# Performance work log

Hardware: AMD Instinct MI355X
Metric: run time of the kernel (lower is better)

## Reference

```python
import jax, jax.numpy as jnp
import numpy as np

N, E, DIM, L, NPERM, B = 20000, 640000, 128, 4, 20000, 256
R = NPERM * L * L  # rows of perm matrices
EPS = 1e-5


def _mlp(x, w1, b1, g, beta, w2, b2):
    # Linear -> BatchNorm (training-mode batch stats) -> ReLU -> Linear
    h = x @ w1 + b1
    mu = h.mean(0)
    var = h.var(0)  # biased, matches torch BN normalization
    h = (h - mu) * jax.lax.rsqrt(var + EPS) * g + beta
    return jax.nn.relu(h) @ w2 + b2


def setup_inputs() -> dict:
    key = jax.random.key(0)
    ks = jax.random.split(key, 40)
    s = 0.05
    inp = {}
    inp["node_feat"] = jax.random.normal(ks[0], (N, DIM), jnp.float32)
    inp["edge_feat"] = jax.random.normal(ks[1], (E, DIM), jnp.float32)
    inp["src"] = jax.random.randint(ks[2], (E,), 0, N)
    inp["dst"] = jax.random.randint(ks[3], (E,), 0, N)
    inp["rev_flag"] = jax.random.randint(ks[4], (E,), 0, 2).astype(bool)
    # sparse node_to_perm / edge_to_perm: one nnz per row (row i implicit)
    inp["n2p_cols"] = jax.random.randint(ks[5], (R,), 0, N)
    inp["n2p_vals"] = jax.random.uniform(ks[6], (R,), jnp.float32)
    inp["e2p_cols"] = jax.random.randint(ks[7], (R,), 0, E)
    inp["e2p_vals"] = jax.random.uniform(ks[8], (R,), jnp.float32)
    # sparse pooling matrix: perm j -> graph pool_rows[j] with weight pool_vals[j]
    inp["pool_rows"] = jax.random.randint(ks[9], (NPERM,), 0, B)
    inp["pool_vals"] = jax.random.uniform(ks[10], (NPERM,), jnp.float32)
    for i, n in enumerate(["in_w", "out_w", "src_w", "dst_w", "nloop_w", "eloop_w"]):
        inp[n] = jax.random.normal(ks[11 + i], (DIM, DIM), jnp.float32) * s
    inp["lrp_w"] = jax.random.normal(ks[17], (DIM, DIM, L * L), jnp.float32) * s
    inp["nbias"] = jnp.zeros((DIM,), jnp.float32)
    inp["ebias"] = jnp.zeros((DIM,), jnp.float32)
    inp["lrp_bias"] = jnp.zeros((DIM,), jnp.float32)
    for p, k0 in (("n", 20), ("e", 26)):
        inp[p + "mlp_w1"] = jax.random.normal(ks[k0], (DIM, DIM), jnp.float32) * s
        inp[p + "mlp_b1"] = jnp.zeros((DIM,), jnp.float32)
        inp[p + "mlp_g"] = jnp.ones((DIM,), jnp.float32)
        inp[p + "mlp_beta"] = jnp.zeros((DIM,), jnp.float32)
        inp[p + "mlp_w2"] = jax.random.normal(ks[k0 + 1], (DIM, DIM), jnp.float32) * s
        inp[p + "mlp_b2"] = jnp.zeros((DIM,), jnp.float32)
    return inp


def reference(node_feat, edge_feat, src, dst, rev_flag, n2p_cols, n2p_vals,
              e2p_cols, e2p_vals, pool_rows, pool_vals,
              in_w, out_w, src_w, dst_w, nloop_w, eloop_w, lrp_w,
              nbias, ebias, lrp_bias,
              nmlp_w1, nmlp_b1, nmlp_g, nmlp_beta, nmlp_w2, nmlp_b2,
              emlp_w1, emlp_b1, emlp_g, emlp_beta, emlp_w2, emlp_b2):
    hs = node_feat[src]   # [E, d]
    hd = node_feat[dst]   # [E, d]
    r = rev_flag[:, None]
    # per-edge messages with reverse-edge masking
    edge_msg = jnp.where(r, hs @ dst_w - hd @ src_w, hd @ dst_w - hs @ src_w)
    node_msg = jnp.where(r, edge_feat @ out_w, -(edge_feat @ in_w))
    node_agg = jax.ops.segment_sum(node_msg, dst, num_segments=N)
    # node update
    nout = _mlp(node_feat @ nloop_w + node_agg + nbias,
                nmlp_w1, nmlp_b1, nmlp_g, nmlp_beta, nmlp_w2, nmlp_b2)
    # edge update: degree-scaled term uses out-degree of dst node
    out_deg = jax.ops.segment_sum(jnp.ones((E,), jnp.float32), src, num_segments=N)
    dlog = jnp.log2(1.0 + out_deg[dst])[:, None]
    add = 2.0 * (1.0 + dlog) * (edge_feat @ (src_w - dst_w))
    eout = _mlp(edge_feat @ eloop_w + add + edge_msg + ebias,
                emlp_w1, emlp_b1, emlp_g, emlp_beta, emlp_w2, emlp_b2)
    # sparse perm gathers + LRP einsum + sparse pooling scatter
    perm = n2p_vals[:, None] * nout[n2p_cols] + e2p_vals[:, None] * eout[e2p_cols]
    perm = perm.reshape(NPERM, L * L, DIM)
    lrp = jnp.einsum('dab,bca->dc', perm, lrp_w) + lrp_bias
    pooled = jax.ops.segment_sum(pool_vals[:, None] * lrp, pool_rows, num_segments=B)
    return pooled, eout
```

## Files before the change

kernel.cpp:

```cpp
#include <hip/hip_runtime.h>
#include <stdint.h>

constexpr int Nn     = 20000;
constexpr int Ee     = 640000;
constexpr int NPERMc = 20000;

using bf16x8 = __attribute__((ext_vector_type(8))) short;
using f32x4  = __attribute__((ext_vector_type(4))) float;
using s16x4  = __attribute__((ext_vector_type(4))) short;
using u16x8  = __attribute__((ext_vector_type(8))) unsigned short;

__device__ __forceinline__ short f2bf(float f) {
  union { float f; unsigned u; } v; v.f = f;
  unsigned r = v.u + 0x7FFFu + ((v.u >> 16) & 1u);
  return (short)(r >> 16);
}
__device__ __forceinline__ float bf2f(unsigned short s) {
  union { unsigned u; float f; } v; v.u = ((unsigned)s) << 16;
  return v.f;
}
__device__ __forceinline__ f32x4 MFMA(bf16x8 a, bf16x8 b, f32x4 c) {
  return __builtin_amdgcn_mfma_f32_16x16x32_bf16(a, b, c, 0, 0, 0);
}

__device__ __forceinline__ int swz(int s) { return s ^ (((s >> 7) & 7) << 3); }

__device__ __forceinline__ int fragIdx(int k, int n) {
  int t = n >> 4, kk = k >> 5;
  int l = ((k & 31) >> 3) * 16 + (n & 15);
  int j = k & 7;
  return ((t * 4 + kk) * 64 + l) * 8 + j;
}

__device__ __forceinline__ void stage16x128(const float* __restrict__ src, int row0, int M,
                                            int lane, short* lds) {
  #pragma unroll
  for (int it = 0; it < 8; ++it) {
    int u = it * 64 + lane;
    int r = u >> 5;
    int q = u & 31;
    int row = row0 + r;
    float4 v = make_float4(0.f, 0.f, 0.f, 0.f);
    if (row < M) v = ((const float4*)(src + (size_t)row * 128))[q];
    int k  = q * 4;
    int kk = k >> 5;
    int l2 = ((k & 31) >> 3) * 16 + r;
    int j  = k & 7;
    s16x4 s4 = { f2bf(v.x), f2bf(v.y), f2bf(v.z), f2bf(v.w) };
    *(s16x4*)(lds + swz((kk * 64 + l2) * 8 + j)) = s4;
  }
}

__global__ __launch_bounds__(256) void kPrep(
    const float* __restrict__ in_w,  const float* __restrict__ out_w,
    const float* __restrict__ src_w, const float* __restrict__ dst_w,
    const float* __restrict__ nloop_w, const float* __restrict__ eloop_w,
    const float* __restrict__ lrp_w,
    const float* __restrict__ nbias, const float* __restrict__ ebias,
    const float* __restrict__ w1e, const float* __restrict__ b1e,
    const float* __restrict__ w1n, const float* __restrict__ b1n,
    const float* __restrict__ w2e, const float* __restrict__ w2n,
    short* __restrict__ WA, short* __restrict__ BQ, short* __restrict__ WN,
    short* __restrict__ W2E, short* __restrict__ W2N, short* __restrict__ WL,
    float* __restrict__ c0e, float* __restrict__ c0n) {
  __shared__ float Rl[16384];
  int tid = threadIdx.x;
  int blk = blockIdx.x;
  if (blk < 448) {
    int p = blk >> 6, sub = blk & 63;
    const float* La; const float* Lb = nullptr; const float* R; short* outp;
    float sOut = 1.f;
    switch (p) {
      case 0: La = eloop_w;             R = w1e; outp = WA;          break;
      case 1: La = src_w; Lb = dst_w;   R = w1e; outp = WA + 16384;  break;
      case 2: La = dst_w;               R = w1e; outp = BQ;          break;
      case 3: La = src_w;               R = w1e; outp = BQ + 16384;  break;
      case 4: La = nloop_w;             R = w1n; outp = WN;          break;
      case 5: La = out_w;               R = w1n; outp = WN + 16384;  break;
      default: La = in_w;               R = w1n; outp = WN + 32768; sOut = -1.f; break;
    }
    for (int i = tid; i < 16384; i += 256) Rl[i] = R[i];
    __syncthreads();
    int e = sub * 256 + tid;
    int k = e >> 7, n = e & 127;
    float acc = 0.f;
    bool hasLb = (Lb != nullptr);
    for (int j = 0; j < 128; ++j) {
      float l = La[k * 128 + j];
      if (hasLb) l -= Lb[k * 128 + j];
      acc += l * Rl[j * 128 + n];
    }
    outp[fragIdx(k, n)] = f2bf(acc * sOut);
  } else if (blk < 512) {
    int e = (blk - 448) * 256 + tid; int k = e >> 7, n = e & 127;
    W2E[fragIdx(k, n)] = f2bf(w2e[k * 128 + n]);
  } else if (blk < 576) {
    int e = (blk - 512) * 256 + tid; int k = e >> 7, n = e & 127;
    W2N[fragIdx(k, n)] = f2bf(w2n[k * 128 + n]);
  } else if (blk < 1600) {
    int q = blk - 576; int a = q >> 6;
    int e = (q & 63) * 256 + tid; int k = e >> 7, n = e & 127;
    WL[a * 16384 + fragIdx(k, n)] = f2bf(lrp_w[(k * 128 + n) * 16 + a]);
  } else {
    if (tid < 128) {
      float acc = 0.f;
      for (int k2 = 0; k2 < 128; ++k2) acc += ebias[k2] * w1e[k2 * 128 + tid];
      c0e[tid] = acc + b1e[tid];
    } else {
      int n = tid - 128; float acc = 0.f;
      for (int k2 = 0; k2 < 128; ++k2) acc += nbias[k2] * w1n[k2 * 128 + n];
      c0n[n] = acc + b1n[n];
    }
  }
}


__global__ __launch_bounds__(256) void kHist(
    const int* __restrict__ srcI, const int* __restrict__ dstI,
    int* __restrict__ cnt, float* __restrict__ deg) {
  int e = blockIdx.x * 256 + threadIdx.x;
  atomicAdd(&cnt[dstI[e]], 1);
  atomicAdd(&deg[srcI[e]], 1.0f);
}

__global__ __launch_bounds__(256) void kScan(const int* __restrict__ cnt,
                                             int* __restrict__ off,
                                             int* __restrict__ cur) {
  __shared__ int lc[Nn];
  __shared__ int ps[256];
  int tid = threadIdx.x;
  for (int i = tid; i < Nn; i += 256) lc[i] = cnt[i];
  __syncthreads();
  constexpr int CH = (Nn + 255) / 256;
  int base = tid * CH;
  int local = 0;
  for (int i = 0; i < CH; ++i) {
    int idx = base + i;
    if (idx < Nn) local += lc[idx];
  }
  ps[tid] = local;
  __syncthreads();
  for (int d = 1; d < 256; d <<= 1) {
    int t = (tid >= d) ? ps[tid - d] : 0;
    __syncthreads();
    if (tid >= d) ps[tid] += t;
    __syncthreads();
  }
  int run = ps[tid] - local;
  for (int i = 0; i < CH; ++i) {
    int idx = base + i;
    if (idx < Nn) { off[idx] = run; cur[idx] = run; run += lc[idx]; }
  }
}

__global__ __launch_bounds__(256) void kScatter(
    const int* __restrict__ dstI, const int* __restrict__ revI,
    int* __restrict__ cur, int* __restrict__ order) {
  int e = blockIdx.x * 256 + threadIdx.x;
  int pos = atomicAdd(&cur[dstI[e]], 1);
  order[pos] = revI[e] ? (e | (int)0x80000000) : e;
}

__global__ __launch_bounds__(256) void kAgg2(
    const float* __restrict__ ef, const int* __restrict__ off,
    const int* __restrict__ cnt, const int* __restrict__ order,
    float* __restrict__ aggR, float* __restrict__ aggN) {
  int w = threadIdx.x >> 6, lane = threadIdx.x & 63;
  int n = blockIdx.x * 4 + w;
  if (n >= Nn) return;
  int s0 = off[n], c = cnt[n];
  float2 aR = make_float2(0.f, 0.f), aN = make_float2(0.f, 0.f);
  int i = 0;
  for (; i + 3 < c; i += 4) {
    int oe0 = order[s0 + i];
    int oe1 = order[s0 + i + 1];
    int oe2 = order[s0 + i + 2];
    int oe3 = order[s0 + i + 3];
    float2 v0 = ((const float2*)(ef + (size_t)(oe0 & 0x7fffffff) * 128))[lane];
    float2 v1 = ((const float2*)(ef + (size_t)(oe1 & 0x7fffffff) * 128))[lane];
    float2 v2 = ((const float2*)(ef + (size_t)(oe2 & 0x7fffffff) * 128))[lane];
    float2 v3 = ((const float2*)(ef + (size_t)(oe3 & 0x7fffffff) * 128))[lane];
    if (oe0 < 0) { aR.x += v0.x; aR.y += v0.y; } else { aN.x += v0.x; aN.y += v0.y; }
    if (oe1 < 0) { aR.x += v1.x; aR.y += v1.y; } else { aN.x += v1.x; aN.y += v1.y; }
    if (oe2 < 0) { aR.x += v2.x; aR.y += v2.y; } else { aN.x += v2.x; aN.y += v2.y; }
    if (oe3 < 0) { aR.x += v3.x; aR.y += v3.y; } else { aN.x += v3.x; aN.y += v3.y; }
  }
  for (; i < c; ++i) {
    int oe = order[s0 + i];
    int e = oe & 0x7fffffff;
    float2 v = ((const float2*)(ef + (size_t)e * 128))[lane];
    if (oe < 0) { aR.x += v.x; aR.y += v.y; } else { aN.x += v.x; aN.y += v.y; }
  }
  ((float2*)(aggR + (size_t)n * 128))[lane] = aR;
  ((float2*)(aggN + (size_t)n * 128))[lane] = aN;
}

__global__ __launch_bounds__(256, 2) void kQ(const float* __restrict__ nf,
                                             const short* __restrict__ BQ,
                                             float* __restrict__ Q, int M) {
  __shared__ __align__(16) short alds[4][2048];
  __shared__ __align__(16) short wbuf[8192];
  int tid = threadIdx.x, w = tid >> 6, lane = tid & 63;
  int row0 = blockIdx.x * 64 + w * 16;
  stage16x128(nf, row0, M, lane, alds[w]);
  f32x4 acc[16];
  #pragma unroll
  for (int t = 0; t < 16; ++t) acc[t] = (f32x4){0.f, 0.f, 0.f, 0.f};
  const int4* g4 = (const int4*)BQ;
  for (int kk = 0; kk < 4; ++kk) {
    __syncthreads();
    for (int c = tid; c < 1024; c += 256) {
      int t = c >> 6, l = c & 63;
      ((int4*)wbuf)[c] = g4[(t * 4 + kk) * 64 + l];
    }
    __syncthreads();
    bf16x8 a = *(const bf16x8*)(alds[w] + swz((kk * 64 + lane) * 8));
    #pragma unroll
    for (int t = 0; t < 16; ++t) {
      bf16x8 b = *(const bf16x8*)(wbuf + (t * 64 + lane) * 8);
      acc[t] = MFMA(a, b, acc[t]);
    }
  }
  int sub = lane >> 4, m = lane & 15;
  #pragma unroll
  for (int i = 0; i < 4; ++i) {
    int row = row0 + sub * 4 + i;
    if (row < M) {
      #pragma unroll
      for (int h = 0; h < 2; ++h) {
        float4 f0, f1;
        f0.x = acc[h * 8 + 0][i]; f0.y = acc[h * 8 + 1][i];
        f0.z = acc[h * 8 + 2][i]; f0.w = acc[h * 8 + 3][i];
        f1.x = acc[h * 8 + 4][i]; f1.y = acc[h * 8 + 5][i];
        f1.z = acc[h * 8 + 6][i]; f1.w = acc[h * 8 + 7][i];
        float4* dst = (float4*)(Q + (size_t)row * 256 + h * 128 + m * 8);
        dst[0] = f0; dst[1] = f1;
      }
    }
  }
}

__global__ __launch_bounds__(256, 2) void kN1(
    const float* __restrict__ nf, const float* __restrict__ aggR,
    const float* __restrict__ aggN, const short* __restrict__ WN,
    const float* __restrict__ c0n, short* __restrict__ hN,
    float* __restrict__ scratchN, int M) {
  __shared__ __align__(16) short alds[4][2048];
  __shared__ __align__(16) short wlds[16384];
  __shared__ float statsLDS[256];
  int tid = threadIdx.x, w = tid >> 6, lane = tid & 63;
  int m = lane & 15, sub = lane >> 4;
  statsLDS[tid] = 0.f;
  int row0 = blockIdx.x * 64 + w * 16;
  f32x4 acc[8];
  #pragma unroll
  for (int t = 0; t < 8; ++t) acc[t] = (f32x4){0.f, 0.f, 0.f, 0.f};
  for (int s = 0; s < 3; ++s) {
    const float* src = (s == 0) ? nf : ((s == 1) ? aggR : aggN);
    __syncthreads();
    const int4* g4 = (const int4*)(WN + s * 16384);
    for (int c = tid; c < 2048; c += 256) ((int4*)wlds)[c] = g4[c];
    __syncthreads();
    stage16x128(src, row0, M, lane, alds[w]);
    for (int kk = 0; kk < 4; ++kk) {
      bf16x8 a = *(const bf16x8*)(alds[w] + swz((kk * 64 + lane) * 8));
      #pragma unroll
      for (int t = 0; t < 8; ++t) {
        bf16x8 b = *(const bf16x8*)(wlds + ((t * 4 + kk) * 64 + lane) * 8);
        acc[t] = MFMA(a, b, acc[t]);
      }
    }
  }
  float c0v[8];
  #pragma unroll
  for (int t = 0; t < 8; ++t) c0v[t] = c0n[t * 16 + m];
  float ss[8], sq[8];
  #pragma unroll
  for (int t = 0; t < 8; ++t) { ss[t] = 0.f; sq[t] = 0.f; }
  #pragma unroll
  for (int i = 0; i < 4; ++i) {
    int row = row0 + sub * 4 + i;
    if (row < M) {
      bf16x8 pk;
      #pragma unroll
      for (int t = 0; t < 8; ++t) {
        float h = acc[t][i] + c0v[t];
        pk[t] = f2bf(h); ss[t] += h; sq[t] += h * h;
      }
      *(bf16x8*)(hN + (size_t)row * 128 + m * 8) = pk;
    }
  }
  #pragma unroll
  for (int t = 0; t < 8; ++t) {
    float a = ss[t], b = sq[t];
    a += __shfl_xor(a, 16, 64); b += __shfl_xor(b, 16, 64);
    a += __shfl_xor(a, 32, 64); b += __shfl_xor(b, 32, 64);
    if (lane < 16) {
      atomicAdd(&statsLDS[t * 16 + lane], a);
      atomicAdd(&statsLDS[128 + t * 16 + lane], b);
    }
  }
  __syncthreads();
  scratchN[(size_t)tid * gridDim.x + blockIdx.x] = statsLDS[tid];
}

__global__ __launch_bounds__(256, 4) void kD(
    const float* __restrict__ ef, const short* __restrict__ WA,
    const float* __restrict__ Q, const float* __restrict__ c0e,
    const int* __restrict__ srcI, const int* __restrict__ dstI,
    const int* __restrict__ revI, const float* __restrict__ deg,
    short* __restrict__ hE, float* __restrict__ scratchE) {
  __shared__ __align__(16) short alds[4][2048];
  __shared__ __align__(16) short wbuf[8192];
  __shared__ float statsLDS[256];
  int tid = threadIdx.x, w = tid >> 6, lane = tid & 63;
  int m = lane & 15, sub = lane >> 4;
  statsLDS[tid] = 0.f;
  int row0 = blockIdx.x * 64 + w * 16;
  float scl[4]; int qa[4], qb[4];
  #pragma unroll
  for (int i = 0; i < 4; ++i) {
    int e = row0 + sub * 4 + i;
    int s_ = srcI[e], d_ = dstI[e], r_ = revI[e];
    scl[i] = 2.0f * (1.0f + log2f(1.0f + deg[d_]));
    int na = r_ ? s_ : d_;
    int nb = r_ ? d_ : s_;
    qa[i] = na * 256 + m * 8;
    qb[i] = nb * 256 + 128 + m * 8;
  }
  stage16x128(ef, row0, Ee, lane, alds[w]);
  f32x4 acc1[8], acc2[8];
  #pragma unroll
  for (int t = 0; t < 8; ++t) { acc1[t] = (f32x4){0,0,0,0}; acc2[t] = (f32x4){0,0,0,0}; }
  const int4* g4 = (const int4*)WA;
  for (int kk = 0; kk < 4; ++kk) {
    __syncthreads();
    for (int c = tid; c < 1024; c += 256) {
      int mm = c >> 9, t = (c >> 6) & 7, l = c & 63;
      ((int4*)wbuf)[c] = g4[mm * 2048 + (t * 4 + kk) * 64 + l];
    }
    __syncthreads();
    bf16x8 a = *(const bf16x8*)(alds[w] + swz((kk * 64 + lane) * 8));
    #pragma unroll
    for (int t = 0; t < 8; ++t) {
      bf16x8 b1 = *(const bf16x8*)(wbuf + (t * 64 + lane) * 8);
      bf16x8 b2 = *(const bf16x8*)(wbuf + 4096 + (t * 64 + lane) * 8);
      acc1[t] = MFMA(a, b1, acc1[t]);
      acc2[t] = MFMA(a, b2, acc2[t]);
    }
  }
  float c0v[8];
  #pragma unroll
  for (int t = 0; t < 8; ++t) c0v[t] = c0e[t * 16 + m];
  float ss[8], sq[8];
  #pragma unroll
  for (int t = 0; t < 8; ++t) { ss[t] = 0.f; sq[t] = 0.f; }
  #pragma unroll
  for (int i = 0; i < 4; ++i) {
    int e = row0 + sub * 4 + i;
    float4 A0 = ((const float4*)(Q + qa[i]))[0];
    float4 A1 = ((const float4*)(Q + qa[i]))[1];
    float4 B0 = ((const float4*)(Q + qb[i]))[0];
    float4 B1 = ((const float4*)(Q + qb[i]))[1];
    float qv[8] = {A0.x - B0.x, A0.y - B0.y, A0.z - B0.z, A0.w - B0.w,
                   A1.x - B1.x, A1.y - B1.y, A1.z - B1.z, A1.w - B1.w};
    bf16x8 pk;
    #pragma unroll
    for (int t = 0; t < 8; ++t) {
      float h = acc1[t][i] + scl[i] * acc2[t][i] + qv[t] + c0v[t];
      pk[t] = f2bf(h);
      ss[t] += h; sq[t] += h * h;
    }
    *(bf16x8*)(hE + (size_t)e * 128 + m * 8) = pk;
  }
  #pragma unroll
  for (int t = 0; t < 8; ++t) {
    float a = ss[t], b = sq[t];
    a += __shfl_xor(a, 16, 64); b += __shfl_xor(b, 16, 64);
    a += __shfl_xor(a, 32, 64); b += __shfl_xor(b, 32, 64);
    if (lane < 16) {
      atomicAdd(&statsLDS[t * 16 + lane], a);
      atomicAdd(&statsLDS[128 + t * 16 + lane], b);
    }
  }
  __syncthreads();
  scratchE[(size_t)tid * gridDim.x + blockIdx.x] = statsLDS[tid];
}

__global__ __launch_bounds__(256) void kFin(const float* __restrict__ scratch, int NB,
                                            float M, const float* __restrict__ g,
                                            const float* __restrict__ beta,
                                            float* __restrict__ st) {
  __shared__ float red[256];
  __shared__ float red2[256];
  int c = blockIdx.x;
  int tid = threadIdx.x;
  float s = 0.f, q = 0.f;
  for (int i = tid; i < NB; i += 256) {
    s += scratch[(size_t)c * NB + i];
    q += scratch[(size_t)(128 + c) * NB + i];
  }
  red[tid] = s; red2[tid] = q;
  __syncthreads();
  for (int off = 128; off > 0; off >>= 1) {
    if (tid < off) { red[tid] += red[tid + off]; red2[tid] += red2[tid + off]; }
    __syncthreads();
  }
  if (tid == 0) {
    float mu  = red[0] / M;
    float var = red2[0] / M - mu * mu;
    float inv = rsqrtf(var + 1e-5f);
    float sc  = g[c] * inv;
    st[c] = sc;
    st[128 + c] = beta[c] - mu * sc;
  }
}

__global__ __launch_bounds__(256, 2) void kF(const short* __restrict__ h,
                                             const float* __restrict__ st,
                                             const short* __restrict__ w2f,
                                             const float* __restrict__ b2,
                                             float* __restrict__ outp, int M) {
  __shared__ __align__(16) short alds[4][2048];
  __shared__ __align__(16) short wlds[16384];
  int tid = threadIdx.x, w = tid >> 6, lane = tid & 63;
  int m2 = lane & 15;
  for (int c = tid; c < 2048; c += 256) ((int4*)wlds)[c] = ((const int4*)w2f)[c];
  int row0 = blockIdx.x * 64 + w * 16;
  float sc8[8], tb8[8];
  #pragma unroll
  for (int q = 0; q < 8; ++q) {
    int col = q * 16 + m2;
    sc8[q] = st[col]; tb8[q] = st[128 + col];
  }
  #pragma unroll
  for (int it = 0; it < 4; ++it) {
    int r = it * 4 + (lane >> 4);
    int row = row0 + r;
    u16x8 hv = {0, 0, 0, 0, 0, 0, 0, 0};
    if (row < M) hv = *(const u16x8*)(h + (size_t)row * 128 + m2 * 8);
    #pragma unroll
    for (int q = 0; q < 8; ++q) {
      float f = bf2f(hv[q]);
      float v = fmaxf(f * sc8[q] + tb8[q], 0.f);
      int k = q * 16 + m2;
      int kk = k >> 5, l2 = ((k & 31) >> 3) * 16 + r, j = k & 7;
      alds[w][swz((kk * 64 + l2) * 8 + j)] = f2bf(v);
    }
  }
  __syncthreads();
  f32x4 acc[8];
  #pragma unroll
  for (int t = 0; t < 8; ++t) acc[t] = (f32x4){0.f, 0.f, 0.f, 0.f};
  for (int kk = 0; kk < 4; ++kk) {
    bf16x8 a = *(const bf16x8*)(alds[w] + swz((kk * 64 + lane) * 8));
    #pragma unroll
    for (int t = 0; t < 8; ++t) {
      bf16x8 b = *(const bf16x8*)(wlds + ((t * 4 + kk) * 64 + lane) * 8);
      acc[t] = MFMA(a, b, acc[t]);
    }
  }
  int sub = lane >> 4;
  #pragma unroll
  for (int t = 0; t < 8; ++t) {
    int col = t * 16 + (lane & 15);
    float bb = b2[col];
    #pragma unroll
    for (int i = 0; i < 4; ++i) {
      int row = row0 + sub * 4 + i;
      if (row < M) outp[(size_t)row * 128 + col] = acc[t][i] + bb;
    }
  }
}

__global__ __launch_bounds__(256, 2) void kLRP(
    const float* __restrict__ nout, const float* __restrict__ eoutp,
    const int* __restrict__ n2pc, const float* __restrict__ n2pv,
    const int* __restrict__ e2pc, const float* __restrict__ e2pv,
    const int* __restrict__ poolr, const float* __restrict__ poolv,
    const short* __restrict__ WL, const float* __restrict__ lrp_bias,
    float* __restrict__ pooled) {
  __shared__ __align__(16) short alds[4][2048];
  __shared__ __align__(16) short wlds[16384];
  int tid = threadIdx.x, w = tid >> 6, lane = tid & 63;
  int blk = blockIdx.x % 313, g = blockIdx.x / 313;
  int row0 = blk * 64 + w * 16;
  int a0 = g * 4;
  f32x4 acc[8];
  #pragma unroll
  for (int t = 0; t < 8; ++t) acc[t] = (f32x4){0.f, 0.f, 0.f, 0.f};
  for (int a = a0; a < a0 + 4; ++a) {
    __syncthreads();
    const int4* g4 = (const int4*)(WL + a * 16384);
    for (int c = tid; c < 2048; c += 256) ((int4*)wlds)[c] = g4[c];
    __syncthreads();
    #pragma unroll
    for (int it = 0; it < 8; ++it) {
      int u = it * 64 + lane;
      int r = u >> 5;
      int q = u & 31;
      int d = row0 + r;
      float4 v = make_float4(0.f, 0.f, 0.f, 0.f);
      if (d < NPERMc) {
        int i = d * 16 + a;
        int nc = n2pc[i]; float nv = n2pv[i];
        int ec = e2pc[i]; float ev = e2pv[i];
        float4 nr = ((const float4*)(nout  + (size_t)nc * 128))[q];
        float4 er = ((const float4*)(eoutp + (size_t)ec * 128))[q];
        v.x = nv * nr.x + ev * er.x;
        v.y = nv * nr.y + ev * er.y;
        v.z = nv * nr.z + ev * er.z;
        v.w = nv * nr.w + ev * er.w;
      }
      int k  = q * 4;
      int kk = k >> 5;
      int l2 = ((k & 31) >> 3) * 16 + r;
      int j  = k & 7;
      s16x4 s4 = { f2bf(v.x), f2bf(v.y), f2bf(v.z), f2bf(v.w) };
      *(s16x4*)(alds[w] + swz((kk * 64 + l2) * 8 + j)) = s4;
    }
    for (int kk = 0; kk < 4; ++kk) {
      bf16x8 aa = *(const bf16x8*)(alds[w] + swz((kk * 64 + lane) * 8));
      #pragma unroll
      for (int t = 0; t < 8; ++t) {
        bf16x8 b = *(const bf16x8*)(wlds + ((t * 4 + kk) * 64 + lane) * 8);
        acc[t] = MFMA(aa, b, acc[t]);
      }
    }
  }
  int sub = lane >> 4;
  #pragma unroll
  for (int t = 0; t < 8; ++t) {
    int col = t * 16 + (lane & 15);
    float lb = (g == 0) ? lrp_bias[col] : 0.f;
    #pragma unroll
    for (int i = 0; i < 4; ++i) {
      int d = row0 + sub * 4 + i;
      if (d < NPERMc) {
        float val = acc[t][i] + lb;
        atomicAdd(&pooled[poolr[d] * 128 + col], poolv[d] * val);
      }
    }
  }
}

extern "C" void kernel_launch(void* const* d_in, const int* in_sizes, int n_in,
                              void* d_out, int out_size, void* d_ws, size_t ws_size,
                              hipStream_t stream) {
  (void)in_sizes; (void)n_in; (void)out_size; (void)ws_size;
  const float* node_feat = (const float*)d_in[0];
  const float* edge_feat = (const float*)d_in[1];
  const int*   srcI      = (const int*)d_in[2];
  const int*   dstI      = (const int*)d_in[3];
  const int*   revI      = (const int*)d_in[4];
  const int*   n2pc      = (const int*)d_in[5];
  const float* n2pv      = (const float*)d_in[6];
  const int*   e2pc      = (const int*)d_in[7];
  const float* e2pv      = (const float*)d_in[8];
  const int*   poolr     = (const int*)d_in[9];
  const float* poolv     = (const float*)d_in[10];
  const float* in_w      = (const float*)d_in[11];
  const float* out_w     = (const float*)d_in[12];
  const float* src_w     = (const float*)d_in[13];
  const float* dst_w     = (const float*)d_in[14];
  const float* nloop_w   = (const float*)d_in[15];
  const float* eloop_w   = (const float*)d_in[16];
  const float* lrp_w     = (const float*)d_in[17];
  const float* nbias     = (const float*)d_in[18];
  const float* ebias     = (const float*)d_in[19];
  const float* lrp_bias  = (const float*)d_in[20];
  const float* nmlp_w1   = (const float*)d_in[21];
  const float* nmlp_b1   = (const float*)d_in[22];
  const float* nmlp_g    = (const float*)d_in[23];
  const float* nmlp_beta = (const float*)d_in[24];
  const float* nmlp_w2   = (const float*)d_in[25];
  const float* nmlp_b2   = (const float*)d_in[26];
  const float* emlp_w1   = (const float*)d_in[27];
  const float* emlp_b1   = (const float*)d_in[28];
  const float* emlp_g    = (const float*)d_in[29];
  const float* emlp_beta = (const float*)d_in[30];
  const float* emlp_w2   = (const float*)d_in[31];
  const float* emlp_b2   = (const float*)d_in[32];

  float* pooled = (float*)d_out;
  float* eoutp  = (float*)d_out + 32768;

  char* p = (char*)d_ws;
  auto alloc = [&](size_t b) { char* r = p; p += (b + 255) & ~(size_t)255; return r; };
  short* hE   = (short*)alloc((size_t)Ee * 128 * 2);
  float* Qm   = (float*)alloc((size_t)Nn * 256 * 4);
  float* aggR = (float*)alloc((size_t)Nn * 128 * 4);
  float* aggN = (float*)alloc((size_t)Nn * 128 * 4);
  short* hN   = (short*)alloc((size_t)Nn * 128 * 2);
  float* nout = (float*)alloc((size_t)Nn * 128 * 4);
  float* deg  = (float*)alloc((size_t)Nn * 4);
  float* scrE = (float*)alloc((size_t)256 * 10000 * 4);
  float* scrN = (float*)alloc((size_t)256 * 313 * 4);
  float* stE  = (float*)alloc(256 * 4);
  float* stN  = (float*)alloc(256 * 4);
  short* WA   = (short*)alloc(32768 * 2);
  short* BQ   = (short*)alloc(32768 * 2);
  short* WN   = (short*)alloc(49152 * 2);
  short* W2E  = (short*)alloc(16384 * 2);
  short* W2N  = (short*)alloc(16384 * 2);
  short* WL   = (short*)alloc((size_t)16 * 16384 * 2);
  float* c0e  = (float*)alloc(128 * 4);
  float* c0n  = (float*)alloc(128 * 4);
  int*   cnt  = (int*)alloc((size_t)Nn * 4);
  int*   offA = (int*)alloc((size_t)Nn * 4);
  int*   cur  = (int*)alloc((size_t)Nn * 4);
  int*   order= (int*)alloc((size_t)Ee * 4);

  hipMemsetAsync(deg,  0, (size_t)Nn * 4, stream);
  hipMemsetAsync(cnt,  0, (size_t)Nn * 4, stream);
  hipMemsetAsync(pooled, 0, (size_t)32768 * 4, stream);

  kPrep<<<1601, 256, 0, stream>>>(in_w, out_w, src_w, dst_w, nloop_w, eloop_w, lrp_w,
                                  nbias, ebias, emlp_w1, emlp_b1, nmlp_w1, nmlp_b1,
                                  emlp_w2, nmlp_w2, WA, BQ, WN, W2E, W2N, WL, c0e, c0n);
  kHist<<<Ee / 256, 256, 0, stream>>>(srcI, dstI, cnt, deg);
  kScan<<<1, 256, 0, stream>>>(cnt, offA, cur);
  kScatter<<<Ee / 256, 256, 0, stream>>>(dstI, revI, cur, order);
  kAgg2<<<Nn / 4, 256, 0, stream>>>(edge_feat, offA, cnt, order, aggR, aggN);
  kQ<<<313, 256, 0, stream>>>(node_feat, BQ, Qm, Nn);
  kN1<<<313, 256, 0, stream>>>(node_feat, aggR, aggN, WN, c0n, hN, scrN, Nn);
  kD<<<10000, 256, 0, stream>>>(edge_feat, WA, Qm, c0e, srcI, dstI, revI, deg, hE, scrE);
  kFin<<<128, 256, 0, stream>>>(scrE, 10000, (float)Ee, emlp_g, emlp_beta, stE);
  kFin<<<128, 256, 0, stream>>>(scrN, 313, (float)Nn, nmlp_g, nmlp_beta, stN);
  kF<<<10000, 256, 0, stream>>>(hE, stE, W2E, emlp_b2, eoutp, Ee);
  kF<<<313, 256, 0, stream>>>(hN, stN, W2N, nmlp_b2, nout, Nn);
  kLRP<<<1252, 256, 0, stream>>>(nout, eoutp, n2pc, n2pv, e2pc, e2pv,
                                 poolr, poolv, WL, lrp_bias, pooled);
}
```

Before: 1.358 ms.

## Stream weight tiles per k-step in kF/kLRP and restructure BN stat reduction

kF and kLRP now stage only the 8 KB weight slice for each k-step into a small LDS buffer instead of the full 32 KB weight matrix. This cuts LDS use enough to raise the launch bounds occupancy hints (kF 2→6, kLRP 2→4). The cost is extra barriers and repeated global/L2 reads of the weights per k-step. Separately, per-block BN statistics are now written block-major (coalesced) and reduced by a new two-stage kRed+kFin pass instead of strided column reads.

```diff
diff --git a/kernel.cpp b/kernel.cpp
--- a/kernel.cpp
+++ b/kernel.cpp
@@ -301,7 +301,7 @@
     }
   }
   __syncthreads();
-  scratchN[(size_t)tid * gridDim.x + blockIdx.x] = statsLDS[tid];
+  scratchN[(size_t)blockIdx.x * 256 + tid] = statsLDS[tid];
 }
 
 __global__ __launch_bounds__(256, 4) void kD(
@@ -384,10 +384,19 @@
     }
   }
   __syncthreads();
-  scratchE[(size_t)tid * gridDim.x + blockIdx.x] = statsLDS[tid];
-}
-
-__global__ __launch_bounds__(256) void kFin(const float* __restrict__ scratch, int NB,
+  scratchE[(size_t)blockIdx.x * 256 + tid] = statsLDS[tid];
+}
+
+__global__ __launch_bounds__(256) void kRed(const float* __restrict__ scr, int NB,
+                                            float* __restrict__ part) {
+  int tid = threadIdx.x, b = blockIdx.x;
+  float acc = 0.f;
+  for (int r = b; r < NB; r += 64)
+    acc += scr[(size_t)r * 256 + tid];
+  part[b * 256 + tid] = acc;
+}
+
+__global__ __launch_bounds__(256) void kFin(const float* __restrict__ part,
                                             float M, const float* __restrict__ g,
                                             const float* __restrict__ beta,
                                             float* __restrict__ st) {
@@ -396,13 +405,13 @@
   int c = blockIdx.x;
   int tid = threadIdx.x;
   float s = 0.f, q = 0.f;
-  for (int i = tid; i < NB; i += 256) {
-    s += scratch[(size_t)c * NB + i];
-    q += scratch[(size_t)(128 + c) * NB + i];
+  if (tid < 64) {
+    s = part[tid * 256 + c];
+    q = part[tid * 256 + 128 + c];
   }
   red[tid] = s; red2[tid] = q;
   __syncthreads();
-  for (int off = 128; off > 0; off >>= 1) {
+  for (int off = 32; off > 0; off >>= 1) {
     if (tid < off) { red[tid] += red[tid + off]; red2[tid] += red2[tid + off]; }
     __syncthreads();
   }
@@ -416,16 +425,15 @@
   }
 }
 
-__global__ __launch_bounds__(256, 2) void kF(const short* __restrict__ h,
+__global__ __launch_bounds__(256, 6) void kF(const short* __restrict__ h,
                                              const float* __restrict__ st,
                                              const short* __restrict__ w2f,
                                              const float* __restrict__ b2,
                                              float* __restrict__ outp, int M) {
   __shared__ __align__(16) short alds[4][2048];
-  __shared__ __align__(16) short wlds[16384];
+  __shared__ __align__(16) short wbuf[4096];
   int tid = threadIdx.x, w = tid >> 6, lane = tid & 63;
   int m2 = lane & 15;
-  for (int c = tid; c < 2048; c += 256) ((int4*)wlds)[c] = ((const int4*)w2f)[c];
   int row0 = blockIdx.x * 64 + w * 16;
   float sc8[8], tb8[8];
   #pragma unroll
@@ -448,15 +456,21 @@
       alds[w][swz((kk * 64 + l2) * 8 + j)] = f2bf(v);
     }
   }
-  __syncthreads();
   f32x4 acc[8];
   #pragma unroll
   for (int t = 0; t < 8; ++t) acc[t] = (f32x4){0.f, 0.f, 0.f, 0.f};
+  const int4* g4w = (const int4*)w2f;
   for (int kk = 0; kk < 4; ++kk) {
+    __syncthreads();
+    for (int c = tid; c < 512; c += 256) {
+      int t = c >> 6, l = c & 63;
+      ((int4*)wbuf)[c] = g4w[(t * 4 + kk) * 64 + l];
+    }
+    __syncthreads();
     bf16x8 a = *(const bf16x8*)(alds[w] + swz((kk * 64 + lane) * 8));
     #pragma unroll
     for (int t = 0; t < 8; ++t) {
-      bf16x8 b = *(const bf16x8*)(wlds + ((t * 4 + kk) * 64 + lane) * 8);
+      bf16x8 b = *(const bf16x8*)(wbuf + (t * 64 + lane) * 8);
       acc[t] = MFMA(a, b, acc[t]);
     }
   }
@@ -473,7 +487,7 @@
   }
 }
 
-__global__ __launch_bounds__(256, 2) void kLRP(
+__global__ __launch_bounds__(256, 4) void kLRP(
     const float* __restrict__ nout, const float* __restrict__ eoutp,
     const int* __restrict__ n2pc, const float* __restrict__ n2pv,
     const int* __restrict__ e2pc, const float* __restrict__ e2pv,
@@ -481,7 +495,7 @@
     const short* __restrict__ WL, const float* __restrict__ lrp_bias,
     float* __restrict__ pooled) {
   __shared__ __align__(16) short alds[4][2048];
-  __shared__ __align__(16) short wlds[16384];
+  __shared__ __align__(16) short wbuf[4096];
   int tid = threadIdx.x, w = tid >> 6, lane = tid & 63;
   int blk = blockIdx.x % 313, g = blockIdx.x / 313;
   int row0 = blk * 64 + w * 16;
@@ -490,10 +504,6 @@
   #pragma unroll
   for (int t = 0; t < 8; ++t) acc[t] = (f32x4){0.f, 0.f, 0.f, 0.f};
   for (int a = a0; a < a0 + 4; ++a) {
-    __syncthreads();
-    const int4* g4 = (const int4*)(WL + a * 16384);
-    for (int c = tid; c < 2048; c += 256) ((int4*)wlds)[c] = g4[c];
-    __syncthreads();
     #pragma unroll
     for (int it = 0; it < 8; ++it) {
       int u = it * 64 + lane;
@@ -519,11 +529,18 @@
       s16x4 s4 = { f2bf(v.x), f2bf(v.y), f2bf(v.z), f2bf(v.w) };
       *(s16x4*)(alds[w] + swz((kk * 64 + l2) * 8 + j)) = s4;
     }
+    const int4* g4 = (const int4*)(WL + a * 16384);
     for (int kk = 0; kk < 4; ++kk) {
+      __syncthreads();
+      for (int c = tid; c < 512; c += 256) {
+        int t = c >> 6, l = c & 63;
+        ((int4*)wbuf)[c] = g4[(t * 4 + kk) * 64 + l];
+      }
+      __syncthreads();
       bf16x8 aa = *(const bf16x8*)(alds[w] + swz((kk * 64 + lane) * 8));
       #pragma unroll
       for (int t = 0; t < 8; ++t) {
-        bf16x8 b = *(const bf16x8*)(wlds + ((t * 4 + kk) * 64 + lane) * 8);
+        bf16x8 b = *(const bf16x8*)(wbuf + (t * 64 + lane) * 8);
         acc[t] = MFMA(aa, b, acc[t]);
       }
     }
@@ -594,8 +611,10 @@
   short* hN   = (short*)alloc((size_t)Nn * 128 * 2);
   float* nout = (float*)alloc((size_t)Nn * 128 * 4);
   float* deg  = (float*)alloc((size_t)Nn * 4);
-  float* scrE = (float*)alloc((size_t)256 * 10000 * 4);
-  float* scrN = (float*)alloc((size_t)256 * 313 * 4);
+  float* scrE = (float*)alloc((size_t)10000 * 256 * 4);
+  float* scrN = (float*)alloc((size_t)313 * 256 * 4);
+  float* partE= (float*)alloc((size_t)64 * 256 * 4);
+  float* partN= (float*)alloc((size_t)64 * 256 * 4);
   float* stE  = (float*)alloc(256 * 4);
   float* stN  = (float*)alloc(256 * 4);
   short* WA   = (short*)alloc(32768 * 2);
@@ -625,8 +644,10 @@
   kQ<<<313, 256, 0, stream>>>(node_feat, BQ, Qm, Nn);
   kN1<<<313, 256, 0, stream>>>(node_feat, aggR, aggN, WN, c0n, hN, scrN, Nn);
   kD<<<10000, 256, 0, stream>>>(edge_feat, WA, Qm, c0e, srcI, dstI, revI, deg, hE, scrE);
-  kFin<<<128, 256, 0, stream>>>(scrE, 10000, (float)Ee, emlp_g, emlp_beta, stE);
-  kFin<<<128, 256, 0, stream>>>(scrN, 313, (float)Nn, nmlp_g, nmlp_beta, stN);
+  kRed<<<64, 256, 0, stream>>>(scrE, 10000, partE);
+  kRed<<<64, 256, 0, stream>>>(scrN, 313, partN);
+  kFin<<<128, 256, 0, stream>>>(partE, (float)Ee, emlp_g, emlp_beta, stE);
+  kFin<<<128, 256, 0, stream>>>(partN, (float)Nn, nmlp_g, nmlp_beta, stN);
   kF<<<10000, 256, 0, stream>>>(hE, stE, W2E, emlp_b2, eoutp, Ee);
   kF<<<313, 256, 0, stream>>>(hN, stN, W2N, nmlp_b2, nout, Nn);
   kLRP<<<1252, 256, 0, stream>>>(nout, eoutp, n2pc, n2pv, e2pc, e2pv,
```

Result: faster. 1.306 ms (-3.9%).
